# Performance work log

Hardware: AMD Instinct MI355X
Metric: run time of the kernel (lower is better)

## Reference

```python
import jax, jax.numpy as jnp
import numpy as np

B, S, D = 2, 2048, 768
H, DK, F = 12, 64, 3072
LN_EPS = 1e-5


def setup_inputs() -> dict:
    key = jax.random.key(0)
    ks = jax.random.split(key, 8)
    w = lambda k, shape: jax.random.normal(k, shape, dtype=jnp.float32) * 0.02
    return {
        "x": jax.random.normal(ks[0], (B, S, D), dtype=jnp.float32),
        "wq_w": w(ks[1], (H, D, DK)), "wq_b": jnp.zeros((H, DK), jnp.float32),
        "wk_w": w(ks[2], (H, D, DK)), "wk_b": jnp.zeros((H, DK), jnp.float32),
        "wv_w": w(ks[3], (H, D, DK)), "wv_b": jnp.zeros((H, DK), jnp.float32),
        "wo_w": w(ks[4], (H * DK, D)), "wo_b": jnp.zeros((D,), jnp.float32),
        "ln_g": jnp.ones((D,), jnp.float32), "ln_b": jnp.zeros((D,), jnp.float32),
        "w1": w(ks[5], (D, F)), "b1": jnp.zeros((F,), jnp.float32),
        "w2": w(ks[6], (F, D)), "b2": jnp.zeros((D,), jnp.float32),
    }


def layer_norm(x, g, b):
    mu = jnp.mean(x, axis=-1, keepdims=True)
    var = jnp.mean(jnp.square(x - mu), axis=-1, keepdims=True)
    return (x - mu) * jax.lax.rsqrt(var + LN_EPS) * g + b


def reference(x, wq_w, wq_b, wk_w, wk_b, wv_w, wv_b, wo_w, wo_b,
              ln_g, ln_b, w1, b1, w2, b2):
    dk = wq_w.shape[-1]
    x_res = x
    h = layer_norm(x, ln_b=ln_b, g=ln_g, b=ln_b) if False else layer_norm(x, ln_g, ln_b)
    # per-head QKV (all heads batched via einsum): [B,H,S,DK]
    q = jnp.einsum("bsd,hdk->bhsk", h, wq_w) + wq_b[None, :, None, :]
    k = jnp.einsum("bsd,hdk->bhsk", h, wk_w) + wk_b[None, :, None, :]
    v = jnp.einsum("bsd,hdk->bhsk", h, wv_w) + wv_b[None, :, None, :]
    scores = jnp.einsum("bhqk,bhsk->bhqs", q, k) / jnp.sqrt(jnp.float32(dk))
    attn = jax.nn.softmax(scores, axis=-1)
    o = jnp.einsum("bhqs,bhsk->bhqk", attn, v)  # [B,H,S,DK]
    Bx, Hx, Sx, Dkx = o.shape
    o = o.transpose(0, 2, 1, 3).reshape(Bx, Sx, Hx * Dkx)  # concat heads
    y = o @ wo_w + wo_b + x_res  # residual 1
    y_res = y
    z = layer_norm(y, ln_g, ln_b)
    z = jax.nn.gelu(z @ w1 + b1, approximate=False) @ w2 + b2
    return z + y_res
```

## Files before the change

### kernel.cpp

```cpp
#include <hip/hip_runtime.h>
#include <hip/hip_bf16.h>
#include <math.h>

typedef __bf16 bf16_t;
typedef __bf16 bf16x8 __attribute__((ext_vector_type(8)));
typedef __bf16 bf16x4 __attribute__((ext_vector_type(4)));
typedef float f32x4 __attribute__((ext_vector_type(4)));

#define MFMA_B16(a, b, c) __builtin_amdgcn_mfma_f32_16x16x32_bf16((a), (b), (c), 0, 0, 0)

static constexpr int Bn = 2, Sn = 2048, Dn = 768, Hn = 12, Fn = 3072;
static constexpr int NTOK = Bn * Sn;
#define QSCALE 0.18033688011112042f

__device__ __forceinline__ void gl_lds16(const bf16_t* g, void* lds) {
  __builtin_amdgcn_global_load_lds(
      (const __attribute__((address_space(1))) uint32_t*)g,
      (__attribute__((address_space(3))) uint32_t*)lds, 16, 0, 0);
}

__global__ __launch_bounds__(256) void k_prep(const float* __restrict__ wq, const float* __restrict__ wk,
                                              const float* __restrict__ wv, const float* __restrict__ wo,
                                              const float* __restrict__ w1, const float* __restrict__ w2,
                                              const float* __restrict__ bq, const float* __restrict__ bk,
                                              const float* __restrict__ bv,
                                              bf16_t* __restrict__ WqkvT, bf16_t* __restrict__ WoT,
                                              bf16_t* __restrict__ W1T, bf16_t* __restrict__ W2T,
                                              float* __restrict__ QKVB,
                                              const float* __restrict__ x, const float* __restrict__ ln_g,
                                              const float* __restrict__ ln_b, bf16_t* __restrict__ Hbuf) {
  int t = blockIdx.x;
  int tid = threadIdx.x;
  if (t >= 1729) {
    int tok = t - 1729;
    const float* xr = x + (size_t)tok * Dn;
    float v0 = xr[tid], v1 = xr[tid + 256], v2 = xr[tid + 512];
    float s = v0 + v1 + v2;
    float ss = v0 * v0 + v1 * v1 + v2 * v2;
    __shared__ float red[8];
#pragma unroll
    for (int off = 32; off > 0; off >>= 1) {
      s += __shfl_down(s, off);
      ss += __shfl_down(ss, off);
    }
    int w = tid >> 6, l = tid & 63;
    if (l == 0) { red[w] = s; red[4 + w] = ss; }
    __syncthreads();
    s = red[0] + red[1] + red[2] + red[3];
    ss = red[4] + red[5] + red[6] + red[7];
    float mu = s * (1.0f / Dn);
    float var = ss * (1.0f / Dn) - mu * mu;
    float rstd = rsqrtf(var + 1e-5f);
    bf16_t* orow = Hbuf + (size_t)tok * Dn;
    orow[tid]       = (bf16_t)((v0 - mu) * rstd * ln_g[tid]       + ln_b[tid]);
    orow[tid + 256] = (bf16_t)((v1 - mu) * rstd * ln_g[tid + 256] + ln_b[tid + 256]);
    orow[tid + 512] = (bf16_t)((v2 - mu) * rstd * ln_g[tid + 512] + ln_b[tid + 512]);
    return;
  }
  if (t == 1728) {
    for (int i = tid; i < 2304; i += 256)
      QKVB[i] = i < 768 ? bq[i] : (i < 1536 ? bk[i - 768] : bv[i - 1536]);
    return;
  }
  __shared__ float T[64][65];
  const float* src;
  bf16_t* dst;
  int P, Q, tp, tq;
  if (t < 432) {
    int pb = t / 12; tp = t - pb * 12; tq = 0;
    int proj = pb / 12, head = pb - proj * 12;
    src = (proj == 0 ? wq : proj == 1 ? wk : wv) + (size_t)head * 768 * 64;
    dst = WqkvT + (size_t)proj * 589824 + (size_t)head * 64 * 768;
    P = 768; Q = 64;
  } else if (t < 576) {
    int u = t - 432; tp = u / 12; tq = u - tp * 12;
    src = wo; dst = WoT; P = 768; Q = 768;
  } else if (t < 1152) {
    int u = t - 576; tp = u / 48; tq = u - tp * 48;
    src = w1; dst = W1T; P = 768; Q = 3072;
  } else {
    int u = t - 1152; tp = u / 12; tq = u - tp * 12;
    src = w2; dst = W2T; P = 3072; Q = 768;
  }
  int j = tid & 63, i0 = tid >> 6;
#pragma unroll
  for (int i = i0; i < 64; i += 4)
    T[i][j] = src[(size_t)(tp * 64 + i) * Q + tq * 64 + j];
  __syncthreads();
#pragma unroll
  for (int i = i0; i < 64; i += 4)
    dst[(size_t)(tq * 64 + i) * P + tp * 64 + j] = (bf16_t)T[j][i];
}

__global__ __launch_bounds__(256) void k_layernorm(const float* __restrict__ x,
                                                   const float* __restrict__ g,
                                                   const float* __restrict__ bb,
                                                   bf16_t* __restrict__ out) {
  int t = blockIdx.x, tid = threadIdx.x;
  const float* xr = x + (size_t)t * Dn;
  float v0 = xr[tid], v1 = xr[tid + 256], v2 = xr[tid + 512];
  float s = v0 + v1 + v2;
  float ss = v0 * v0 + v1 * v1 + v2 * v2;
  __shared__ float red[8];
#pragma unroll
  for (int off = 32; off > 0; off >>= 1) {
    s += __shfl_down(s, off);
    ss += __shfl_down(ss, off);
  }
  int w = tid >> 6, l = tid & 63;
  if (l == 0) { red[w] = s; red[4 + w] = ss; }
  __syncthreads();
  s = red[0] + red[1] + red[2] + red[3];
  ss = red[4] + red[5] + red[6] + red[7];
  float mu = s * (1.0f / Dn);
  float var = ss * (1.0f / Dn) - mu * mu;
  float rstd = rsqrtf(var + 1e-5f);
  bf16_t* orow = out + (size_t)t * Dn;
  orow[tid]       = (bf16_t)((v0 - mu) * rstd * g[tid]       + bb[tid]);
  orow[tid + 256] = (bf16_t)((v1 - mu) * rstd * g[tid + 256] + bb[tid + 256]);
  orow[tid + 512] = (bf16_t)((v2 - mu) * rstd * g[tid + 512] + bb[tid + 512]);
}

enum { EPI_QK = 0, EPI_VT = 1, EPI_Y = 2, EPI_GELU = 3, EPI_OUT = 4 };

template <int MT, int NT, int BK, int EPI, int OCC, int SWZ>
__global__ __launch_bounds__(256, OCC) void k_gemm(const bf16_t* __restrict__ A,
                                                   const bf16_t* __restrict__ Bt,
                                                   int N, int K,
                                                   const float* __restrict__ bias,
                                                   const float* __restrict__ resid,
                                                   void* __restrict__ out0,
                                                   void* __restrict__ out1) {
  constexpr int MI = MT / 32, NI = NT / 32;
  constexpr int WROWS = MT / 2, WCOLS = NT / 2;
  constexpr int KS = BK / 32;
  __shared__ __align__(16) bf16_t As[2][MT * BK];
  __shared__ __align__(16) bf16_t Bs[2][NT * BK];
  const int tid = threadIdx.x;
  const int w = tid >> 6, l = tid & 63;
  const int wm = w >> 1, wn = w & 1;
  const int mloc = l & 15, kblk = l >> 4;
  int bx = blockIdx.x, by = blockIdx.y;
  if constexpr (SWZ) {
    int lin = by * gridDim.x + bx;
    int xcd = lin & 7, s = lin >> 3;
    by = xcd * (gridDim.y >> 3) + s / gridDim.x;
    bx = s - (s / gridDim.x) * gridDim.x;
  }

  f32x4 acc[MI][NI];
#pragma unroll
  for (int i = 0; i < MI; ++i)
#pragma unroll
    for (int j = 0; j < NI; ++j) acc[i][j] = f32x4{0.f, 0.f, 0.f, 0.f};

  const bf16_t* gA = A + (size_t)(by * MT + (tid >> 2)) * K + (tid & 3) * 8;
  const bf16_t* gB = Bt + (size_t)(bx * NT + (tid >> 2)) * K + (tid & 3) * 8;
  const int nk = K / BK;

  auto stage = [&](int kt, int buf) {
#pragma unroll
    for (int h = 0; h < KS; ++h) {
#pragma unroll
      for (int rb = 0; rb < MT / 64; ++rb)
        gl_lds16(gA + (size_t)rb * 64 * K + kt * BK + h * 32,
                 (char*)&As[buf][0] + h * (MT * 64) + rb * 4096 + w * 1024);
#pragma unroll
      for (int rb = 0; rb < NT / 64; ++rb)
        gl_lds16(gB + (size_t)rb * 64 * K + kt * BK + h * 32,
                 (char*)&Bs[buf][0] + h * (NT * 64) + rb * 4096 + w * 1024);
    }
  };

  stage(0, 0);
  for (int kt = 0; kt < nk; ++kt) {
    __syncthreads();
    if (kt + 1 < nk) stage(kt + 1, (kt + 1) & 1);
    const bf16_t* Ab = &As[kt & 1][0];
    const bf16_t* Bb = &Bs[kt & 1][0];
    bf16x8 af[MI][KS], bfv[NI][KS];
#pragma unroll
    for (int mi = 0; mi < MI; ++mi)
#pragma unroll
      for (int ks = 0; ks < KS; ++ks)
        af[mi][ks] = *(const bf16x8*)&Ab[ks * (MT * 32) + (wm * WROWS + mi * 16 + mloc) * 32 + kblk * 8];
#pragma unroll
    for (int ni = 0; ni < NI; ++ni)
#pragma unroll
      for (int ks = 0; ks < KS; ++ks)
        bfv[ni][ks] = *(const bf16x8*)&Bb[ks * (NT * 32) + (wn * WCOLS + ni * 16 + mloc) * 32 + kblk * 8];
#pragma unroll
    for (int ks = 0; ks < KS; ++ks)
#pragma unroll
      for (int mi = 0; mi < MI; ++mi)
#pragma unroll
        for (int ni = 0; ni < NI; ++ni)
          acc[mi][ni] = MFMA_B16(af[mi][ks], bfv[ni][ks], acc[mi][ni]);
  }

  const int gmb = by * MT + wm * WROWS + kblk * 4;
  const int gnb = bx * NT + wn * WCOLS + mloc;
  if constexpr (EPI == EPI_QK) {
    constexpr int TPP = 768 / NT;
    const int proj = bx / TPP;
#pragma unroll
    for (int mi = 0; mi < MI; ++mi)
#pragma unroll
      for (int ni = 0; ni < NI; ++ni) {
        int gn = gnb + ni * 16;
        float bv = bias[gn];
        int gm0 = gmb + mi * 16;
        if (proj == 0) {
          bf16_t* dst = (bf16_t*)out0;
#pragma unroll
          for (int r = 0; r < 4; ++r)
            dst[(size_t)(gm0 + r) * 768 + gn] = (bf16_t)((acc[mi][ni][r] + bv) * QSCALE);
        } else {
          bf16_t* dst = (bf16_t*)out1;
#pragma unroll
          for (int r = 0; r < 4; ++r)
            dst[(size_t)(gm0 + r) * 768 + (gn - 768)] = (bf16_t)(acc[mi][ni][r] + bv);
        }
      }
  } else if constexpr (EPI == EPI_VT) {
    bf16_t* dst = (bf16_t*)out0;
#pragma unroll
    for (int mi = 0; mi < MI; ++mi)
#pragma unroll
      for (int ni = 0; ni < NI; ++ni) {
        int gn = gnb + ni * 16;
        int bq = gn >> 11, sq = gn & 2047;
#pragma unroll
        for (int r = 0; r < 4; ++r) {
          int gm = gmb + mi * 16 + r;
          int hq = gm >> 6, dk = gm & 63;
          dst[((size_t)(bq * Hn + hq) * 64 + dk) * Sn + sq] = (bf16_t)(acc[mi][ni][r] + bias[gm]);
        }
      }
  } else if constexpr (EPI == EPI_GELU) {
    bf16_t* dst = (bf16_t*)out0;
#pragma unroll
    for (int mi = 0; mi < MI; ++mi)
#pragma unroll
      for (int ni = 0; ni < NI; ++ni) {
        int gn = gnb + ni * 16;
        float bv = bias[gn];
#pragma unroll
        for (int r = 0; r < 4; ++r) {
          int gm = gmb + mi * 16 + r;
          float t = acc[mi][ni][r] + bv;
          float ge = 0.5f * t * (1.0f + erff(t * 0.70710678118654752f));
          dst[(size_t)gm * N + gn] = (bf16_t)ge;
        }
      }
  } else {
    float* dst = (float*)out0;
#pragma unroll
    for (int mi = 0; mi < MI; ++mi)
#pragma unroll
      for (int ni = 0; ni < NI; ++ni) {
        int gn = gnb + ni * 16;
        float bv = bias[gn];
#pragma unroll
        for (int r = 0; r < 4; ++r) {
          int gm = gmb + mi * 16 + r;
          dst[(size_t)gm * N + gn] = acc[mi][ni][r] + bv + resid[(size_t)gm * N + gn];
        }
      }
  }
}

__global__ __launch_bounds__(512, 2) void k_attn(const bf16_t* __restrict__ Q,
                                                 const bf16_t* __restrict__ K,
                                                 const bf16_t* __restrict__ VT,
                                                 bf16_t* __restrict__ O) {
  __shared__ __align__(16) char smem[65536];
  const int tid = threadIdx.x, w = tid >> 6, l = tid & 63;
  const int g = w >> 2, lw = w & 3;
  const int mloc = l & 15, kblk = l >> 4;
  const int bh = blockIdx.y, b = bh / Hn, h = bh - b * Hn;
  const int q0 = blockIdx.x * 128;

  const size_t qoffA = (size_t)(b * Sn + q0 + lw * 32 + mloc) * Dn + h * 64 + kblk * 8;
  const bf16x8 qfa0 = *(const bf16x8*)(Q + qoffA);
  const bf16x8 qfa1 = *(const bf16x8*)(Q + qoffA + 32);
  const bf16x8 qfb0 = *(const bf16x8*)(Q + qoffA + (size_t)16 * Dn);
  const bf16x8 qfb1 = *(const bf16x8*)(Q + qoffA + (size_t)16 * Dn + 32);

  bf16x8 ones;
#pragma unroll
  for (int j = 0; j < 8; ++j) ones[j] = (bf16_t)1.0f;

  const int tq = lw * 16 + (l >> 2);
  const int s0 = (tq & 0x23) | ((tq & 0x0C) << 1) | ((tq & 0x10) >> 2);
  const bf16_t* Kg = K + (size_t)(b * Sn + s0) * Dn + h * 64 + (l & 3) * 8;
  const int c0 = (2 * lw) >> 2, rg0 = (2 * lw) & 3;
  const int c1 = (2 * lw + 1) >> 2, rg1 = (2 * lw + 1) & 3;
  const bf16_t* Vg0 = VT + ((size_t)bh * 64 + rg0 * 16 + (l >> 2)) * Sn + c0 * 32 + (l & 3) * 8;
  const bf16_t* Vg1 = VT + ((size_t)bh * 64 + rg1 * 16 + (l >> 2)) * Sn + c1 * 32 + (l & 3) * 8;

  char* Kbase = smem + g * 16384;
  char* Vbase = smem + 32768 + g * 16384;

  f32x4 lacca = f32x4{0.f, 0.f, 0.f, 0.f};
  f32x4 laccb = f32x4{0.f, 0.f, 0.f, 0.f};
  f32x4 oacca[4], oaccb[4];
#pragma unroll
  for (int md = 0; md < 4; ++md) {
    oacca[md] = f32x4{0.f, 0.f, 0.f, 0.f};
    oaccb[md] = f32x4{0.f, 0.f, 0.f, 0.f};
  }

  auto stage = [&](int tile, int buf) {
    const size_t kv0 = (size_t)tile * 64;
    gl_lds16(Kg + kv0 * Dn,      Kbase + buf * 8192 + lw * 1024);
    gl_lds16(Kg + kv0 * Dn + 32, Kbase + buf * 8192 + 4096 + lw * 1024);
    gl_lds16(Vg0 + kv0, Vbase + buf * 8192 + c0 * 4096 + rg0 * 1024);
    gl_lds16(Vg1 + kv0, Vbase + buf * 8192 + c1 * 4096 + rg1 * 1024);
  };

  constexpr int NIT = Sn / 128;
  stage(g, 0);
  for (int ii = 0; ii < NIT; ++ii) {
    __syncthreads();
    if (ii + 1 < NIT) stage(g + 2 * (ii + 1), (ii + 1) & 1);
    const bf16_t* Kb = (const bf16_t*)(Kbase + (ii & 1) * 8192);
    const bf16_t* Vb = (const bf16_t*)(Vbase + (ii & 1) * 8192);

    f32x4 sa[4], sb[4];
#pragma unroll
    for (int ns = 0; ns < 4; ++ns) {
      const bf16x8 k0 = *(const bf16x8*)&Kb[(ns * 16 + mloc) * 32 + kblk * 8];
      const bf16x8 k1 = *(const bf16x8*)&Kb[2048 + (ns * 16 + mloc) * 32 + kblk * 8];
      f32x4 a = f32x4{0.f, 0.f, 0.f, 0.f};
      a = MFMA_B16(k0, qfa0, a);
      a = MFMA_B16(k1, qfa1, a);
      sa[ns] = a;
      f32x4 c = f32x4{0.f, 0.f, 0.f, 0.f};
      c = MFMA_B16(k0, qfb0, c);
      c = MFMA_B16(k1, qfb1, c);
      sb[ns] = c;
    }

    bf16x8 pa[2], pbv[2];
#pragma unroll
    for (int ns = 0; ns < 4; ++ns)
#pragma unroll
      for (int r = 0; r < 4; ++r) {
        pa[ns >> 1][(ns & 1) * 4 + r]  = (bf16_t)__builtin_amdgcn_exp2f(sa[ns][r]);
        pbv[ns >> 1][(ns & 1) * 4 + r] = (bf16_t)__builtin_amdgcn_exp2f(sb[ns][r]);
      }

#pragma unroll
    for (int c = 0; c < 2; ++c) {
      lacca = MFMA_B16(ones, pa[c], lacca);
      laccb = MFMA_B16(ones, pbv[c], laccb);
    }

#pragma unroll
    for (int md = 0; md < 4; ++md)
#pragma unroll
      for (int c = 0; c < 2; ++c) {
        const bf16x8 v = *(const bf16x8*)&Vb[c * 2048 + (md * 16 + mloc) * 32 + kblk * 8];
        oacca[md] = MFMA_B16(v, pa[c], oacca[md]);
        oaccb[md] = MFMA_B16(v, pbv[c], oaccb[md]);
      }
  }

  __syncthreads();
  float* Red = (float*)smem;
  float* p = Red + (size_t)(lw * 64 + l) * 34;
  if (g == 1) {
#pragma unroll
    for (int md = 0; md < 4; ++md)
#pragma unroll
      for (int r = 0; r < 4; ++r) {
        p[md * 4 + r]      = oacca[md][r];
        p[16 + md * 4 + r] = oaccb[md][r];
      }
    p[32] = lacca[0];
    p[33] = laccb[0];
  }
  __syncthreads();
  if (g == 0) {
#pragma unroll
    for (int md = 0; md < 4; ++md)
#pragma unroll
      for (int r = 0; r < 4; ++r) {
        oacca[md][r] += p[md * 4 + r];
        oaccb[md][r] += p[16 + md * 4 + r];
      }
    const float invA = 1.0f / (lacca[0] + p[32]);
    const float invB = 1.0f / (laccb[0] + p[33]);
    const size_t obA = (size_t)(b * Sn + q0 + lw * 32 + mloc) * Dn + h * 64 + kblk * 4;
    const size_t obB = obA + (size_t)16 * Dn;
#pragma unroll
    for (int md = 0; md < 4; ++md) {
      bf16x4 oa, ob;
#pragma unroll
      for (int r = 0; r < 4; ++r) {
        oa[r] = (bf16_t)(oacca[md][r] * invA);
        ob[r] = (bf16_t)(oaccb[md][r] * invB);
      }
      *(bf16x4*)&O[obA + md * 16] = oa;
      *(bf16x4*)&O[obB + md * 16] = ob;
    }
  }
}

extern "C" void kernel_launch(void* const* d_in, const int* in_sizes, int n_in,
                              void* d_out, int out_size, void* d_ws, size_t ws_size,
                              hipStream_t stream) {
  (void)in_sizes; (void)n_in; (void)out_size; (void)ws_size;
  const float* x    = (const float*)d_in[0];
  const float* wq_w = (const float*)d_in[1];
  const float* wq_b = (const float*)d_in[2];
  const float* wk_w = (const float*)d_in[3];
  const float* wk_b = (const float*)d_in[4];
  const float* wv_w = (const float*)d_in[5];
  const float* wv_b = (const float*)d_in[6];
  const float* wo_w = (const float*)d_in[7];
  const float* wo_b = (const float*)d_in[8];
  const float* ln_g = (const float*)d_in[9];
  const float* ln_b = (const float*)d_in[10];
  const float* w1   = (const float*)d_in[11];
  const float* b1   = (const float*)d_in[12];
  const float* w2   = (const float*)d_in[13];
  const float* b2   = (const float*)d_in[14];

  char* ws = (char*)d_ws;
  size_t o = 0;
  bf16_t* WqkvT = (bf16_t*)(ws + o); o += (size_t)2304 * 768 * 2;
  bf16_t* WoT   = (bf16_t*)(ws + o); o += (size_t)768 * 768 * 2;
  bf16_t* W1T   = (bf16_t*)(ws + o); o += (size_t)3072 * 768 * 2;
  bf16_t* W2T   = (bf16_t*)(ws + o); o += (size_t)768 * 3072 * 2;
  float*  QKVB  = (float*)(ws + o);  o += (size_t)2304 * 4;
  bf16_t* Hbuf  = (bf16_t*)(ws + o); o += (size_t)NTOK * 768 * 2;
  bf16_t* Qb    = (bf16_t*)(ws + o); o += (size_t)NTOK * 768 * 2;
  bf16_t* Kb    = (bf16_t*)(ws + o); o += (size_t)NTOK * 768 * 2;
  bf16_t* VbT   = (bf16_t*)(ws + o); o += (size_t)NTOK * 768 * 2;
  float*  Ybuf  = (float*)(ws + o);  o += (size_t)NTOK * 768 * 4;
  bf16_t* Zbuf  = (bf16_t*)(ws + o); o += (size_t)NTOK * 768 * 2;
  bf16_t* Ubuf  = (bf16_t*)(ws + o); o += (size_t)NTOK * 3072 * 2;

  k_prep<<<1729 + NTOK, 256, 0, stream>>>(wq_w, wk_w, wv_w, wo_w, w1, w2,
                                          wq_b, wk_b, wv_b, WqkvT, WoT, W1T, W2T, QKVB,
                                          x, ln_g, ln_b, Hbuf);

  k_gemm<128, 64, 64, EPI_QK, 3, 1><<<dim3(24, 32), 256, 0, stream>>>(Hbuf, WqkvT, 1536, 768,
                                                                      QKVB, nullptr, Qb, Kb);

  k_gemm<64, 64, 64, EPI_VT, 4, 0><<<dim3(64, 12), 256, 0, stream>>>(WqkvT + (size_t)2 * 589824, Hbuf,
                                                                     4096, 768, QKVB + 1536, nullptr,
                                                                     VbT, nullptr);

  k_attn<<<dim3(Sn / 128, Bn * Hn), 512, 0, stream>>>(Qb, Kb, VbT, Hbuf);

  k_gemm<64, 64, 64, EPI_Y, 4, 1><<<dim3(12, 64), 256, 0, stream>>>(Hbuf, WoT, 768, 768,
                                                                    wo_b, x, Ybuf, nullptr);

  k_layernorm<<<NTOK, 256, 0, stream>>>(Ybuf, ln_g, ln_b, Zbuf);

  k_gemm<128, 128, 32, EPI_GELU, 3, 1><<<dim3(24, 32), 256, 0, stream>>>(Zbuf, W1T, 3072, 768,
                                                                         b1, nullptr, Ubuf, nullptr);

  k_gemm<64, 64, 64, EPI_OUT, 4, 1><<<dim3(12, 64), 256, 0, stream>>>(Ubuf, W2T, 768, 3072,
                                                                      b2, Ybuf, d_out, nullptr);
}
```

Baseline: 265.6 us.

## Split-K the FFN down-projection with atomic accumulation and retile the up-projection

The layernorm kernel now also writes residual plus b2 into the output buffer, so the down-projection GEMM can run split-K across two slices and atomically add its partial sums there. That GEMM moves to 128x64 tiles with a z-dimension of 2, and the GELU up-projection changes from 128x128/BK32 to 128x64/BK64 tiles. The aim is more blocks in flight and better occupancy on the two FFN GEMMs. In exchange it adds atomic traffic on the output and makes fp32 summation order nondeterministic.

```diff
diff --git a/kernel.cpp b/kernel.cpp
--- a/kernel.cpp
+++ b/kernel.cpp
@@ -95,7 +95,9 @@
 __global__ __launch_bounds__(256) void k_layernorm(const float* __restrict__ x,
                                                    const float* __restrict__ g,
                                                    const float* __restrict__ bb,
-                                                   bf16_t* __restrict__ out) {
+                                                   bf16_t* __restrict__ out,
+                                                   const float* __restrict__ b2,
+                                                   float* __restrict__ dinit) {
   int t = blockIdx.x, tid = threadIdx.x;
   const float* xr = x + (size_t)t * Dn;
   float v0 = xr[tid], v1 = xr[tid + 256], v2 = xr[tid + 512];
@@ -119,11 +121,15 @@
   orow[tid]       = (bf16_t)((v0 - mu) * rstd * g[tid]       + bb[tid]);
   orow[tid + 256] = (bf16_t)((v1 - mu) * rstd * g[tid + 256] + bb[tid + 256]);
   orow[tid + 512] = (bf16_t)((v2 - mu) * rstd * g[tid + 512] + bb[tid + 512]);
-}
-
-enum { EPI_QK = 0, EPI_VT = 1, EPI_Y = 2, EPI_GELU = 3, EPI_OUT = 4 };
-
-template <int MT, int NT, int BK, int EPI, int OCC, int SWZ>
+  float* drow = dinit + (size_t)t * Dn;
+  drow[tid]       = v0 + b2[tid];
+  drow[tid + 256] = v1 + b2[tid + 256];
+  drow[tid + 512] = v2 + b2[tid + 512];
+}
+
+enum { EPI_QK = 0, EPI_VT = 1, EPI_Y = 2, EPI_GELU = 3, EPI_OUTA = 4 };
+
+template <int MT, int NT, int BK, int EPI, int OCC, int SWZ, int KSPLIT = 1>
 __global__ __launch_bounds__(256, OCC) void k_gemm(const bf16_t* __restrict__ A,
                                                    const bf16_t* __restrict__ Bt,
                                                    int N, int K,
@@ -147,6 +153,7 @@
     by = xcd * (gridDim.y >> 3) + s / gridDim.x;
     bx = s - (s / gridDim.x) * gridDim.x;
   }
+  const int kof = (KSPLIT > 1) ? blockIdx.z * (K / KSPLIT) : 0;
 
   f32x4 acc[MI][NI];
 #pragma unroll
@@ -154,9 +161,9 @@
 #pragma unroll
     for (int j = 0; j < NI; ++j) acc[i][j] = f32x4{0.f, 0.f, 0.f, 0.f};
 
-  const bf16_t* gA = A + (size_t)(by * MT + (tid >> 2)) * K + (tid & 3) * 8;
-  const bf16_t* gB = Bt + (size_t)(bx * NT + (tid >> 2)) * K + (tid & 3) * 8;
-  const int nk = K / BK;
+  const bf16_t* gA = A + (size_t)(by * MT + (tid >> 2)) * K + kof + (tid & 3) * 8;
+  const bf16_t* gB = Bt + (size_t)(bx * NT + (tid >> 2)) * K + kof + (tid & 3) * 8;
+  const int nk = K / BK / KSPLIT;
 
   auto stage = [&](int kt, int buf) {
 #pragma unroll
@@ -251,6 +258,19 @@
           float t = acc[mi][ni][r] + bv;
           float ge = 0.5f * t * (1.0f + erff(t * 0.70710678118654752f));
           dst[(size_t)gm * N + gn] = (bf16_t)ge;
+        }
+      }
+  } else if constexpr (EPI == EPI_OUTA) {
+    float* dst = (float*)out0;
+#pragma unroll
+    for (int mi = 0; mi < MI; ++mi)
+#pragma unroll
+      for (int ni = 0; ni < NI; ++ni) {
+        int gn = gnb + ni * 16;
+#pragma unroll
+        for (int r = 0; r < 4; ++r) {
+          int gm = gmb + mi * 16 + r;
+          atomicAdd(&dst[(size_t)gm * N + gn], acc[mi][ni][r]);
         }
       }
   } else {
@@ -459,11 +479,11 @@
   k_gemm<64, 64, 64, EPI_Y, 4, 1><<<dim3(12, 64), 256, 0, stream>>>(Hbuf, WoT, 768, 768,
                                                                     wo_b, x, Ybuf, nullptr);
 
-  k_layernorm<<<NTOK, 256, 0, stream>>>(Ybuf, ln_g, ln_b, Zbuf);
-
-  k_gemm<128, 128, 32, EPI_GELU, 3, 1><<<dim3(24, 32), 256, 0, stream>>>(Zbuf, W1T, 3072, 768,
-                                                                         b1, nullptr, Ubuf, nullptr);
-
-  k_gemm<64, 64, 64, EPI_OUT, 4, 1><<<dim3(12, 64), 256, 0, stream>>>(Ubuf, W2T, 768, 3072,
-                                                                      b2, Ybuf, d_out, nullptr);
-}
+  k_layernorm<<<NTOK, 256, 0, stream>>>(Ybuf, ln_g, ln_b, Zbuf, b2, (float*)d_out);
+
+  k_gemm<128, 64, 64, EPI_GELU, 3, 1><<<dim3(48, 32), 256, 0, stream>>>(Zbuf, W1T, 3072, 768,
+                                                                        b1, nullptr, Ubuf, nullptr);
+
+  k_gemm<128, 64, 64, EPI_OUTA, 3, 1, 2><<<dim3(12, 32, 2), 256, 0, stream>>>(Ubuf, W2T, 768, 3072,
+                                                                              nullptr, nullptr, d_out, nullptr);
+}
```

Result: slower. 278.2 us (+4.7%).
